# Kernel optimization log

Hardware: AMD Instinct MI355X
Metric: run time of the kernel (lower is better)

## Reference

```python
import jax, jax.numpy as jnp
import numpy as np

B, S, D_IN, D_OUT = 4, 2048, 1024, 1024

def setup_inputs() -> dict:
    key = jax.random.key(0)
    kx, kq, kk, kv = jax.random.split(key, 4)
    sc = 1.0 / np.sqrt(D_IN)
    x = jax.random.normal(kx, (B, S, D_IN), dtype=jnp.float32)
    Wq = jax.random.normal(kq, (D_IN, D_OUT), dtype=jnp.float32) * sc
    Wk = jax.random.normal(kk, (D_IN, D_OUT), dtype=jnp.float32) * sc
    Wv = jax.random.normal(kv, (D_IN, D_OUT), dtype=jnp.float32) * sc
    return {"x": x, "Wq": Wq, "Wk": Wk, "Wv": Wv}

def reference(x, Wq, Wk, Wv):
    # x: [B,S,Din]; projections to [B,S,Dout]
    q = jnp.einsum('bsd,de->bse', x, Wq)
    k = jnp.einsum('bsd,de->bse', x, Wk)
    v = jnp.einsum('bsd,de->bse', x, Wv)
    scale = 1.0 / jnp.sqrt(jnp.asarray(q.shape[-1], q.dtype))
    scores = jnp.einsum('bqe,bke->bqk', q, k) * scale  # [B,S,S]
    causal = jnp.tril(jnp.ones((scores.shape[-2], scores.shape[-1]), dtype=bool))
    scores = jnp.where(causal, scores, -jnp.inf)
    attn = jax.nn.softmax(scores, axis=-1)
    # dropout p=0.0 -> identity
    return jnp.einsum('bqk,bke->bqe', attn, v)
```

## Files before the change

kernel.cpp:

```cpp
#include <hip/hip_runtime.h>

#define SEQ 2048
#define DIM 1024

typedef __attribute__((ext_vector_type(8))) __bf16 bf16x8;
typedef __attribute__((ext_vector_type(4))) float f32x4;

typedef __attribute__((address_space(1))) unsigned char gu8_t;
typedef __attribute__((address_space(3))) unsigned char lu8_t;

__device__ __forceinline__ void async_copy16(const void* g, void* l) {
  __builtin_amdgcn_global_load_lds((gu8_t*)g, (lu8_t*)l, 16, 0, 0);
}

__device__ __forceinline__ ushort f2bf(float f) {
  union { float f; unsigned u; } v;
  v.f = f;
  unsigned r = v.u + 0x7FFFu + ((v.u >> 16) & 1u);
  return (ushort)(r >> 16);
}

__global__ void prep(const void* __restrict__ xin, const void* __restrict__ w0,
                     const void* __restrict__ w1, const void* __restrict__ w2,
                     ushort* __restrict__ xb, ushort* __restrict__ wt,
                     int* __restrict__ flag, float* __restrict__ lsum) {
  __shared__ ushort tile[64][68];
  __shared__ int redi[4];
  const int bid = blockIdx.x;
  const int t = threadIdx.x;

  const unsigned wv = ((const unsigned*)xin)[t];
  const unsigned b = (wv >> 8) & 0x7Fu;
  int hits = (b >= 0x3Bu && b <= 0x42u) ? 1 : 0;
#pragma unroll
  for (int o = 32; o > 0; o >>= 1) hits += __shfl_xor(hits, o, 64);
  if ((t & 63) == 0) redi[t >> 6] = hits;
  __syncthreads();
  const int bf = (redi[0] + redi[1] + redi[2] + redi[3] > 128) ? 1 : 0;

  if (bid >= 1280) {
    reinterpret_cast<float4*>(lsum)[(bid - 1280) * 256 + t] =
        make_float4(0.f, 0.f, 0.f, 0.f);
    if (bid == 1280 && t == 0) *flag = bf;
    return;
  }

  if (bid < 512) {
#pragma unroll
    for (int j = 0; j < 8; j++) {
      const int i = bid * 2048 + j * 256 + t;
      if (bf) {
        reinterpret_cast<uint4*>(xb)[i] =
            reinterpret_cast<const uint4*>(xin)[i];
      } else {
        const float4* f = reinterpret_cast<const float4*>(xin);
        const float4 a = f[2 * i], bb = f[2 * i + 1];
        ushort4 lo, hi;
        lo.x = f2bf(a.x); lo.y = f2bf(a.y); lo.z = f2bf(a.z); lo.w = f2bf(a.w);
        hi.x = f2bf(bb.x); hi.y = f2bf(bb.y); hi.z = f2bf(bb.z);
        hi.w = f2bf(bb.w);
        reinterpret_cast<ushort4*>(xb)[2 * i] = lo;
        reinterpret_cast<ushort4*>(xb)[2 * i + 1] = hi;
      }
    }
    return;
  }

  const int rem = bid - 512;
  const int z = rem >> 8;
  const int within = rem & 255;
  const int c0 = (within & 15) * 64, r0 = (within >> 4) * 64;
  const void* in = (z == 0) ? w0 : (z == 1) ? w1 : w2;
  ushort* op = wt + (size_t)z * 1024 * 1024;

  if (bf) {
    const ushort* ip = (const ushort*)in;
#pragma unroll
    for (int i = 0; i < 4; i++) {
      const int lin = i * 256 + t;
      const int r = lin >> 4, c4 = (lin & 15) << 2;
      const ushort4 v = *reinterpret_cast<const ushort4*>(
          ip + (size_t)(r0 + r) * 1024 + c0 + c4);
      tile[r][c4 + 0] = v.x; tile[r][c4 + 1] = v.y;
      tile[r][c4 + 2] = v.z; tile[r][c4 + 3] = v.w;
    }
  } else {
    const float* ip = (const float*)in;
#pragma unroll
    for (int i = 0; i < 4; i++) {
      const int lin = i * 256 + t;
      const int r = lin >> 4, c4 = (lin & 15) << 2;
      const float4 v = *reinterpret_cast<const float4*>(
          ip + (size_t)(r0 + r) * 1024 + c0 + c4);
      tile[r][c4 + 0] = f2bf(v.x); tile[r][c4 + 1] = f2bf(v.y);
      tile[r][c4 + 2] = f2bf(v.z); tile[r][c4 + 3] = f2bf(v.w);
    }
  }
  __syncthreads();
#pragma unroll
  for (int i = 0; i < 4; i++) {
    const int lin = i * 256 + t;
    const int c = lin >> 4, r4 = (lin & 15) << 2;
    ushort4 v;
    v.x = tile[r4 + 0][c]; v.y = tile[r4 + 1][c];
    v.z = tile[r4 + 2][c]; v.w = tile[r4 + 3][c];
    *reinterpret_cast<ushort4*>(op + (size_t)(c0 + c) * 1024 + r0 + r4) = v;
  }
}

template <int MODE>
__global__ __launch_bounds__(512, 2) void gemm8(
    const ushort* __restrict__ p0, const ushort* __restrict__ p1,
    const ushort* __restrict__ p2, void* __restrict__ c0,
    void* __restrict__ c1, float* __restrict__ lsum) {
  __shared__ ushort sA[2][2][128 * 64];
  __shared__ ushort sB[2][2][128 * 64];

  const ushort* A;
  const ushort* B;
  ushort* C;
  float* ls = nullptr;
  int m0, n0;
  long ldA, ldB, ldC;
  float scale = 1.0f;
  bool isE = false;

  const int id = blockIdx.x;
  if constexpr (MODE == 0) {
    const int z = id >> 7, r = id & 127;
    m0 = (r >> 2) << 8;
    n0 = (r & 3) << 8;
    A = p0; ldA = 1024;
    B = p1 + (size_t)z * 1024 * 1024; ldB = 1024;
    C = (ushort*)c0 + (size_t)z * 8192 * 1024; ldC = 1024;
    scale = z ? 1.0f : 0.03125f;
  } else {
    if (id < 144) {
      isE = true;
      const int z = id / 36;
      const int tri = id % 36;
      int mt = 0;
      while ((mt + 1) * (mt + 2) / 2 <= tri) mt++;
      const int nt = tri - mt * (mt + 1) / 2;
      m0 = mt << 8;
      n0 = nt << 8;
      A = p0 + (size_t)z * SEQ * DIM; ldA = 1024;
      B = p0 + (size_t)8192 * 1024 + (size_t)z * SEQ * DIM; ldB = 1024;
      C = (ushort*)c0 + (size_t)z * SEQ * SEQ; ldC = 2048;
      ls = lsum + (size_t)z * SEQ;
    } else {
      const int r = id - 144;
      m0 = (r >> 5) << 8;
      n0 = (r & 31) << 8;
      A = p1 + 2 * 1024 * 1024; ldA = 1024;
      B = p2; ldB = 1024;
      C = (ushort*)c1; ldC = 8192;
    }
  }
  constexpr int nT = 16;

  const int tid = threadIdx.x;
  const int lane = tid & 63;
  const int w = tid >> 6;
  const int quad = lane >> 4;
  const int l15 = lane & 15;
  const int ah = w >> 2;
  const int wn = (w & 3) << 6;
  const int bh = wn >> 7;
  const int bo = wn & 64;

  const ushort* aSrc[2][2];
  const ushort* bSrc[2][2];
#pragma unroll
  for (int h = 0; h < 2; h++)
#pragma unroll
    for (int i = 0; i < 2; i++) {
      const int g = i * 512 + tid;
      const int rl = g >> 3;
      const int ck = (g & 7) ^ (rl & 7);
      aSrc[h][i] = A + (size_t)(m0 + h * 128 + rl) * ldA + ck * 8;
      bSrc[h][i] = B + (size_t)(n0 + h * 128 + rl) * ldB + ck * 8;
    }

  auto stageA = [&](int t, int b) {
#pragma unroll
    for (int h = 0; h < 2; h++)
#pragma unroll
      for (int i = 0; i < 2; i++)
        async_copy16(aSrc[h][i] + t * 64, &sA[b][h][(i * 512 + tid) * 8]);
  };
  auto stageB = [&](int t, int b) {
#pragma unroll
    for (int h = 0; h < 2; h++)
#pragma unroll
      for (int i = 0; i < 2; i++)
        async_copy16(bSrc[h][i] + t * 64, &sB[b][h][(i * 512 + tid) * 8]);
  };
  auto rdA = [&](int b, int rbase, int kh) -> bf16x8 {
    const int row = rbase + l15;
    const int ck = ((kh << 2) | quad) ^ (row & 7);
    return *(const bf16x8*)&sA[b][ah][row * 64 + ck * 8];
  };
  auto rdB = [&](int b, int rbase, int kh) -> bf16x8 {
    const int row = rbase + l15;
    const int ck = ((kh << 2) | quad) ^ (row & 7);
    return *(const bf16x8*)&sB[b][bh][row * 64 + ck * 8];
  };

  f32x4 acc[8][4] = {};
  bf16x8 aF[8], bF0[4], bF1[4];

  stageA(0, 0); stageB(0, 0);
  stageA(1, 1); stageB(1, 1);
  asm volatile("s_waitcnt vmcnt(8)" ::: "memory");
  __builtin_amdgcn_s_barrier();

#pragma unroll 1
  for (int t = 0; t < nT; t++) {
    const int b = t & 1;

#pragma unroll
    for (int m = 0; m < 4; m++)
#pragma unroll
      for (int h = 0; h < 2; h++) aF[m * 2 + h] = rdA(b, m * 16, h);
#pragma unroll
    for (int n = 0; n < 2; n++)
#pragma unroll
      for (int h = 0; h < 2; h++) bF0[n * 2 + h] = rdB(b, bo + n * 16, h);
    __builtin_amdgcn_s_barrier();
    __builtin_amdgcn_s_setprio(1);
#pragma unroll
    for (int h = 0; h < 2; h++)
#pragma unroll
      for (int m = 0; m < 4; m++)
#pragma unroll
        for (int n = 0; n < 2; n++)
          acc[m][n] = __builtin_amdgcn_mfma_f32_16x16x32_bf16(
              aF[m * 2 + h], bF0[n * 2 + h], acc[m][n], 0, 0, 0);
    __builtin_amdgcn_s_setprio(0);
    __builtin_amdgcn_s_barrier();

#pragma unroll
    for (int n = 0; n < 2; n++)
#pragma unroll
      for (int h = 0; h < 2; h++)
        bF1[n * 2 + h] = rdB(b, bo + 32 + n * 16, h);
    __builtin_amdgcn_s_barrier();
    __builtin_amdgcn_s_setprio(1);
#pragma unroll
    for (int h = 0; h < 2; h++)
#pragma unroll
      for (int m = 0; m < 4; m++)
#pragma unroll
        for (int n = 0; n < 2; n++)
          acc[m][2 + n] = __builtin_amdgcn_mfma_f32_16x16x32_bf16(
              aF[m * 2 + h], bF1[n * 2 + h], acc[m][2 + n], 0, 0, 0);
    __builtin_amdgcn_s_setprio(0);
    __builtin_amdgcn_s_barrier();

#pragma unroll
    for (int m = 0; m < 4; m++)
#pragma unroll
      for (int h = 0; h < 2; h++) aF[m * 2 + h] = rdA(b, 64 + m * 16, h);
    if (t + 2 < nT) stageB(t + 2, b);
    __builtin_amdgcn_s_barrier();
    __builtin_amdgcn_s_setprio(1);
#pragma unroll
    for (int h = 0; h < 2; h++)
#pragma unroll
      for (int m = 0; m < 4; m++)
#pragma unroll
        for (int n = 0; n < 2; n++)
          acc[4 + m][n] = __builtin_amdgcn_mfma_f32_16x16x32_bf16(
              aF[m * 2 + h], bF0[n * 2 + h], acc[4 + m][n], 0, 0, 0);
    __builtin_amdgcn_s_setprio(0);
    __builtin_amdgcn_s_barrier();

    if (t + 2 < nT) stageA(t + 2, b);
    __builtin_amdgcn_s_setprio(1);
#pragma unroll
    for (int h = 0; h < 2; h++)
#pragma unroll
      for (int m = 0; m < 4; m++)
#pragma unroll
        for (int n = 0; n < 2; n++)
          acc[4 + m][2 + n] = __builtin_amdgcn_mfma_f32_16x16x32_bf16(
              aF[m * 2 + h], bF1[n * 2 + h], acc[4 + m][2 + n], 0, 0, 0);
    __builtin_amdgcn_s_setprio(0);
    if (t + 2 < nT)
      asm volatile("s_waitcnt vmcnt(8)" ::: "memory");
    else
      asm volatile("s_waitcnt vmcnt(0)" ::: "memory");
    __builtin_amdgcn_s_barrier();
  }

  if (MODE == 1 && isE) {
#pragma unroll
    for (int mi = 0; mi < 8; mi++)
#pragma unroll
      for (int r = 0; r < 4; r++) {
        const int row = m0 + ah * 128 + mi * 16 + quad * 4 + r;
        float partial = 0.0f;
#pragma unroll
        for (int ni = 0; ni < 4; ni++) {
          const int col = n0 + wn + ni * 16 + l15;
          const float ev = (col <= row) ? __expf(acc[mi][ni][r]) : 0.0f;
          C[(size_t)row * ldC + col] = f2bf(ev);
          partial += ev;
        }
#pragma unroll
        for (int o = 1; o < 16; o <<= 1) partial += __shfl_xor(partial, o, 64);
        if (l15 == 0) atomicAdd(&ls[row], partial);
      }
  } else {
#pragma unroll
    for (int mi = 0; mi < 8; mi++)
#pragma unroll
      for (int ni = 0; ni < 4; ni++)
#pragma unroll
        for (int r = 0; r < 4; r++) {
          const int row = m0 + ah * 128 + mi * 16 + quad * 4 + r;
          const int col = n0 + wn + ni * 16 + l15;
          C[(size_t)row * ldC + col] = f2bf(acc[mi][ni][r] * scale);
        }
  }
}

template <int EPI, int OUTK, int CK, int SWIZ, int M, int N, int K, long AZ,
          long BZ, long CZ, long BRS>
__global__ __launch_bounds__(256, 4) void gemm_t(
    const ushort* __restrict__ A, const ushort* __restrict__ Bt,
    void* __restrict__ Cv, const int* __restrict__ flag,
    float* __restrict__ lsum, float scale0, float scale1) {
  __shared__ ushort lA[128 * 64];
  __shared__ ushort lB[128 * 64];
  __shared__ float lsh[(EPI == 2) ? 128 : 1];

  constexpr int MT = M / 128;
  const int nT = gridDim.x;
  const int id = blockIdx.y * nT + blockIdx.x;
  const int xcd = id & 7;
  const int loc = id >> 3;
  int nt, mt;
  if constexpr (SWIZ == 1) {
    const int ng = nT >> 3;
    nt = xcd * ng + loc % ng;
    mt = loc / ng;
  } else if constexpr (SWIZ == 2) {
    if (loc <= xcd) { mt = xcd; nt = loc; }
    else { mt = MT - 1 - xcd; nt = loc - xcd - 1; }
  } else if constexpr (SWIZ == 3) {
    nt = xcd;
    mt = loc;
  } else {
    nt = loc % nT;
    mt = xcd + ((loc / nT) << 3);
  }
  const int n0 = nt * 128;
  const int m0 = mt * 128;

  const int z = blockIdx.z;
  const ushort* Ab = A + (size_t)z * AZ;
  const ushort* Bb = Bt + (size_t)z * BZ;

  const int t = threadIdx.x;
  const int lane = t & 63;
  const int w = t >> 6;
  const int wm = (w >> 1) * 64;
  const int wn = (w & 1) * 64;
  const int quad = lane >> 4;
  const int l15 = lane & 15;

  if constexpr (EPI == 2) {
    if (t < 128) lsh[t] = 1.0f / lsum[(size_t)z * M + m0 + t];
  }

  f32x4 acc[4][4] = {};

  const int kEnd = CK ? ((m0 + 128 < K) ? (m0 + 128) : K) : K;

  for (int k0 = 0; k0 < kEnd; k0 += 64) {
    __syncthreads();
#pragma unroll
    for (int g0 = 0; g0 < 1024; g0 += 256) {
      const int g = g0 + t;
      const int r = g >> 3, c = (g & 7) << 3;
      async_copy16(Ab + (size_t)(m0 + r) * K + k0 + c, lA + g * 8);
    }
#pragma unroll
    for (int g0 = 0; g0 < 1024; g0 += 256) {
      const int g = g0 + t;
      const int r = g >> 3, c = (g & 7) << 3;
      async_copy16(Bb + (size_t)(n0 + r) * BRS + k0 + c, lB + g * 8);
    }
    __syncthreads();

#pragma unroll
    for (int h = 0; h < 2; h++) {
      bf16x8 af[4], bfr[4];
#pragma unroll
      for (int mi = 0; mi < 4; mi++)
        af[mi] = *(const bf16x8*)(lA + (wm + mi * 16 + l15) * 64 + h * 32 +
                                  quad * 8);
#pragma unroll
      for (int ni = 0; ni < 4; ni++)
        bfr[ni] = *(const bf16x8*)(lB + (wn + ni * 16 + l15) * 64 + h * 32 +
                                   quad * 8);
#pragma unroll
      for (int mi = 0; mi < 4; mi++)
#pragma unroll
        for (int ni = 0; ni < 4; ni++)
          acc[mi][ni] = __builtin_amdgcn_mfma_f32_16x16x32_bf16(
              af[mi], bfr[ni], acc[mi][ni], 0, 0, 0);
    }
  }

  const size_t zc = (size_t)z * CZ;

  if constexpr (EPI == 1) {
    ushort* C = (ushort*)Cv + zc;
    float* ls = lsum + (size_t)z * M;
#pragma unroll
    for (int mi = 0; mi < 4; mi++)
#pragma unroll
      for (int r = 0; r < 4; r++) {
        const int row = m0 + wm + mi * 16 + quad * 4 + r;
        float partial = 0.0f;
#pragma unroll
        for (int ni = 0; ni < 4; ni++) {
          const int col = n0 + wn + ni * 16 + l15;
          const float ev = (col <= row) ? __expf(acc[mi][ni][r]) : 0.0f;
          C[(size_t)row * N + col] = f2bf(ev);
          partial += ev;
        }
#pragma unroll
        for (int o = 1; o < 16; o <<= 1) partial += __shfl_xor(partial, o, 64);
        if (l15 == 0) atomicAdd(&ls[row], partial);
      }
    return;
  } else {
    const float scale = (z == 0) ? scale0 : scale1;
    const bool storeBf = (OUTK == 1) || (OUTK == 2 && *flag != 0);
#pragma unroll
    for (int mi = 0; mi < 4; mi++)
#pragma unroll
      for (int ni = 0; ni < 4; ni++)
#pragma unroll
        for (int r = 0; r < 4; r++) {
          const int lrow = wm + mi * 16 + quad * 4 + r;
          const int row = m0 + lrow;
          const int col = n0 + wn + ni * 16 + l15;
          const float sc = (EPI == 2) ? lsh[lrow] : scale;
          const float vv = acc[mi][ni][r] * sc;
          if (storeBf) {
            ushort* C = (ushort*)Cv + zc;
            C[(size_t)row * N + col] = f2bf(vv);
          } else {
            float* C = (float*)Cv + zc;
            C[(size_t)row * N + col] = vv;
          }
        }
  }
}

extern "C" void kernel_launch(void* const* d_in, const int* in_sizes, int n_in,
                              void* d_out, int out_size, void* d_ws,
                              size_t ws_size, hipStream_t stream) {
  char* ws = (char*)d_ws;
  const size_t MB = 1024 * 1024;
  int* flag = (int*)ws;
  ushort* wt = (ushort*)(ws + 1 * MB);
  ushort* xb = (ushort*)(ws + 7 * MB);
  ushort* q = (ushort*)(ws + 23 * MB);
  ushort* vt = (ushort*)(ws + 55 * MB);
  ushort* sc = (ushort*)(ws + 71 * MB);
  float* lsum = (float*)(ws + 103 * MB);

  prep<<<dim3(1288), 256, 0, stream>>>(d_in[0], d_in[1], d_in[2], d_in[3], xb,
                                       wt, flag, lsum);

  gemm8<0><<<dim3(256), 512, 0, stream>>>(xb, wt, nullptr, (void*)q, nullptr,
                                          nullptr);

  gemm8<1><<<dim3(272), 512, 0, stream>>>(q, wt, xb, (void*)sc, (void*)vt,
                                          lsum);

  gemm_t<2, 2, 1, 3, 2048, 1024, 2048, (long)SEQ * SEQ, 2048L,
         (long)SEQ * DIM, 8192L>
      <<<dim3(8, 16, 4), 256, 0, stream>>>(sc, vt, d_out, flag, lsum, 1.0f,
                                           1.0f);
}
```

Before: 242.0 us.

## Fuse prep and two GEMM launches into one cooperative kernel with grid syncs

New measurement: 520.8 us. +115.2%, slower.

```diff
diff --git a/kernel.cpp b/kernel.cpp
--- a/kernel.cpp
+++ b/kernel.cpp
@@ -1,4 +1,7 @@
 #include <hip/hip_runtime.h>
+#include <hip/hip_cooperative_groups.h>
+
+namespace cg = cooperative_groups;
 
 #define SEQ 2048
 #define DIM 1024
@@ -20,143 +23,14 @@
   return (ushort)(r >> 16);
 }
 
-__global__ void prep(const void* __restrict__ xin, const void* __restrict__ w0,
-                     const void* __restrict__ w1, const void* __restrict__ w2,
-                     ushort* __restrict__ xb, ushort* __restrict__ wt,
-                     int* __restrict__ flag, float* __restrict__ lsum) {
-  __shared__ ushort tile[64][68];
-  __shared__ int redi[4];
-  const int bid = blockIdx.x;
-  const int t = threadIdx.x;
-
-  const unsigned wv = ((const unsigned*)xin)[t];
-  const unsigned b = (wv >> 8) & 0x7Fu;
-  int hits = (b >= 0x3Bu && b <= 0x42u) ? 1 : 0;
-#pragma unroll
-  for (int o = 32; o > 0; o >>= 1) hits += __shfl_xor(hits, o, 64);
-  if ((t & 63) == 0) redi[t >> 6] = hits;
-  __syncthreads();
-  const int bf = (redi[0] + redi[1] + redi[2] + redi[3] > 128) ? 1 : 0;
-
-  if (bid >= 1280) {
-    reinterpret_cast<float4*>(lsum)[(bid - 1280) * 256 + t] =
-        make_float4(0.f, 0.f, 0.f, 0.f);
-    if (bid == 1280 && t == 0) *flag = bf;
-    return;
-  }
-
-  if (bid < 512) {
-#pragma unroll
-    for (int j = 0; j < 8; j++) {
-      const int i = bid * 2048 + j * 256 + t;
-      if (bf) {
-        reinterpret_cast<uint4*>(xb)[i] =
-            reinterpret_cast<const uint4*>(xin)[i];
-      } else {
-        const float4* f = reinterpret_cast<const float4*>(xin);
-        const float4 a = f[2 * i], bb = f[2 * i + 1];
-        ushort4 lo, hi;
-        lo.x = f2bf(a.x); lo.y = f2bf(a.y); lo.z = f2bf(a.z); lo.w = f2bf(a.w);
-        hi.x = f2bf(bb.x); hi.y = f2bf(bb.y); hi.z = f2bf(bb.z);
-        hi.w = f2bf(bb.w);
-        reinterpret_cast<ushort4*>(xb)[2 * i] = lo;
-        reinterpret_cast<ushort4*>(xb)[2 * i + 1] = hi;
-      }
-    }
-    return;
-  }
-
-  const int rem = bid - 512;
-  const int z = rem >> 8;
-  const int within = rem & 255;
-  const int c0 = (within & 15) * 64, r0 = (within >> 4) * 64;
-  const void* in = (z == 0) ? w0 : (z == 1) ? w1 : w2;
-  ushort* op = wt + (size_t)z * 1024 * 1024;
-
-  if (bf) {
-    const ushort* ip = (const ushort*)in;
-#pragma unroll
-    for (int i = 0; i < 4; i++) {
-      const int lin = i * 256 + t;
-      const int r = lin >> 4, c4 = (lin & 15) << 2;
-      const ushort4 v = *reinterpret_cast<const ushort4*>(
-          ip + (size_t)(r0 + r) * 1024 + c0 + c4);
-      tile[r][c4 + 0] = v.x; tile[r][c4 + 1] = v.y;
-      tile[r][c4 + 2] = v.z; tile[r][c4 + 3] = v.w;
-    }
-  } else {
-    const float* ip = (const float*)in;
-#pragma unroll
-    for (int i = 0; i < 4; i++) {
-      const int lin = i * 256 + t;
-      const int r = lin >> 4, c4 = (lin & 15) << 2;
-      const float4 v = *reinterpret_cast<const float4*>(
-          ip + (size_t)(r0 + r) * 1024 + c0 + c4);
-      tile[r][c4 + 0] = f2bf(v.x); tile[r][c4 + 1] = f2bf(v.y);
-      tile[r][c4 + 2] = f2bf(v.z); tile[r][c4 + 3] = f2bf(v.w);
-    }
-  }
-  __syncthreads();
-#pragma unroll
-  for (int i = 0; i < 4; i++) {
-    const int lin = i * 256 + t;
-    const int c = lin >> 4, r4 = (lin & 15) << 2;
-    ushort4 v;
-    v.x = tile[r4 + 0][c]; v.y = tile[r4 + 1][c];
-    v.z = tile[r4 + 2][c]; v.w = tile[r4 + 3][c];
-    *reinterpret_cast<ushort4*>(op + (size_t)(c0 + c) * 1024 + r0 + r4) = v;
-  }
-}
-
-template <int MODE>
-__global__ __launch_bounds__(512, 2) void gemm8(
-    const ushort* __restrict__ p0, const ushort* __restrict__ p1,
-    const ushort* __restrict__ p2, void* __restrict__ c0,
-    void* __restrict__ c1, float* __restrict__ lsum) {
-  __shared__ ushort sA[2][2][128 * 64];
-  __shared__ ushort sB[2][2][128 * 64];
-
-  const ushort* A;
-  const ushort* B;
-  ushort* C;
-  float* ls = nullptr;
-  int m0, n0;
-  long ldA, ldB, ldC;
-  float scale = 1.0f;
-  bool isE = false;
-
-  const int id = blockIdx.x;
-  if constexpr (MODE == 0) {
-    const int z = id >> 7, r = id & 127;
-    m0 = (r >> 2) << 8;
-    n0 = (r & 3) << 8;
-    A = p0; ldA = 1024;
-    B = p1 + (size_t)z * 1024 * 1024; ldB = 1024;
-    C = (ushort*)c0 + (size_t)z * 8192 * 1024; ldC = 1024;
-    scale = z ? 1.0f : 0.03125f;
-  } else {
-    if (id < 144) {
-      isE = true;
-      const int z = id / 36;
-      const int tri = id % 36;
-      int mt = 0;
-      while ((mt + 1) * (mt + 2) / 2 <= tri) mt++;
-      const int nt = tri - mt * (mt + 1) / 2;
-      m0 = mt << 8;
-      n0 = nt << 8;
-      A = p0 + (size_t)z * SEQ * DIM; ldA = 1024;
-      B = p0 + (size_t)8192 * 1024 + (size_t)z * SEQ * DIM; ldB = 1024;
-      C = (ushort*)c0 + (size_t)z * SEQ * SEQ; ldC = 2048;
-      ls = lsum + (size_t)z * SEQ;
-    } else {
-      const int r = id - 144;
-      m0 = (r >> 5) << 8;
-      n0 = (r & 31) << 8;
-      A = p1 + 2 * 1024 * 1024; ldA = 1024;
-      B = p2; ldB = 1024;
-      C = (ushort*)c1; ldC = 8192;
-    }
-  }
+__device__ __forceinline__ void gemm_core(
+    const ushort* __restrict__ A, const ushort* __restrict__ B,
+    ushort* __restrict__ C, float* __restrict__ ls, const bool isE,
+    const int m0, const int n0, const long ldA, const long ldB,
+    const long ldC, const float scale) {
+  __shared__ ushort sA[2][2][8192];
+  __shared__ ushort sB[2][2][8192];
+
   constexpr int nT = 16;
 
   const int tid = threadIdx.x;
@@ -294,7 +168,7 @@
     __builtin_amdgcn_s_barrier();
   }
 
-  if (MODE == 1 && isE) {
+  if (isE) {
 #pragma unroll
     for (int mi = 0; mi < 8; mi++)
 #pragma unroll
@@ -323,6 +197,138 @@
           const int col = n0 + wn + ni * 16 + l15;
           C[(size_t)row * ldC + col] = f2bf(acc[mi][ni][r] * scale);
         }
+  }
+}
+
+__global__ __launch_bounds__(512, 2) void fused(
+    const void* __restrict__ xin, const void* __restrict__ w0,
+    const void* __restrict__ w1, const void* __restrict__ w2,
+    ushort* __restrict__ xb, ushort* __restrict__ wt, int* __restrict__ flag,
+    float* __restrict__ lsum, ushort* __restrict__ q, ushort* __restrict__ sc,
+    ushort* __restrict__ vt) {
+  __shared__ ushort tile[64][68];
+  __shared__ int redi[8];
+  const int bid = blockIdx.x;
+  const int tid = threadIdx.x;
+  cg::grid_group grid = cg::this_grid();
+
+  {
+    const unsigned wv = ((const unsigned*)xin)[tid];
+    const unsigned b1 = (wv >> 8) & 0x7Fu;
+    int hits = (b1 >= 0x3Bu && b1 <= 0x42u) ? 1 : 0;
+#pragma unroll
+    for (int o = 32; o > 0; o >>= 1) hits += __shfl_xor(hits, o, 64);
+    if ((tid & 63) == 0) redi[tid >> 6] = hits;
+  }
+  __syncthreads();
+  int hsum = 0;
+#pragma unroll
+  for (int i = 0; i < 8; i++) hsum += redi[i];
+  const int bf = (hsum > 256) ? 1 : 0;
+
+  if (bid == 0 && tid == 0) *flag = bf;
+  if (bid < 4)
+    reinterpret_cast<float4*>(lsum)[bid * 512 + tid] =
+        make_float4(0.f, 0.f, 0.f, 0.f);
+
+  if (bf) {
+#pragma unroll
+    for (int j = 0; j < 8; j++) {
+      const int i = bid * 4096 + j * 512 + tid;
+      reinterpret_cast<uint4*>(xb)[i] = reinterpret_cast<const uint4*>(xin)[i];
+    }
+  } else {
+#pragma unroll
+    for (int j = 0; j < 8; j++) {
+      const int i = bid * 4096 + j * 512 + tid;
+      const float4* f = reinterpret_cast<const float4*>(xin);
+      const float4 a = f[2 * i], bb = f[2 * i + 1];
+      ushort4 lo, hi;
+      lo.x = f2bf(a.x); lo.y = f2bf(a.y); lo.z = f2bf(a.z); lo.w = f2bf(a.w);
+      hi.x = f2bf(bb.x); hi.y = f2bf(bb.y); hi.z = f2bf(bb.z);
+      hi.w = f2bf(bb.w);
+      reinterpret_cast<ushort4*>(xb)[2 * i] = lo;
+      reinterpret_cast<ushort4*>(xb)[2 * i + 1] = hi;
+    }
+  }
+
+#pragma unroll 1
+  for (int tt = 0; tt < 3; tt++) {
+    const int rem = bid * 3 + tt;
+    const int z = rem >> 8;
+    const int within = rem & 255;
+    const int c0 = (within & 15) * 64, r0 = (within >> 4) * 64;
+    const void* in = (z == 0) ? w0 : (z == 1) ? w1 : w2;
+    ushort* op = wt + (size_t)z * 1048576;
+
+    __syncthreads();
+    if (bf) {
+      const ushort* ip = (const ushort*)in;
+#pragma unroll
+      for (int i = 0; i < 2; i++) {
+        const int lin = i * 512 + tid;
+        const int r = lin >> 4, c4 = (lin & 15) << 2;
+        const ushort4 v = *reinterpret_cast<const ushort4*>(
+            ip + (size_t)(r0 + r) * 1024 + c0 + c4);
+        tile[r][c4 + 0] = v.x; tile[r][c4 + 1] = v.y;
+        tile[r][c4 + 2] = v.z; tile[r][c4 + 3] = v.w;
+      }
+    } else {
+      const float* ip = (const float*)in;
+#pragma unroll
+      for (int i = 0; i < 2; i++) {
+        const int lin = i * 512 + tid;
+        const int r = lin >> 4, c4 = (lin & 15) << 2;
+        const float4 v = *reinterpret_cast<const float4*>(
+            ip + (size_t)(r0 + r) * 1024 + c0 + c4);
+        tile[r][c4 + 0] = f2bf(v.x); tile[r][c4 + 1] = f2bf(v.y);
+        tile[r][c4 + 2] = f2bf(v.z); tile[r][c4 + 3] = f2bf(v.w);
+      }
+    }
+    __syncthreads();
+#pragma unroll
+    for (int i = 0; i < 2; i++) {
+      const int lin = i * 512 + tid;
+      const int c = lin >> 4, r4 = (lin & 15) << 2;
+      ushort4 v;
+      v.x = tile[r4 + 0][c]; v.y = tile[r4 + 1][c];
+      v.z = tile[r4 + 2][c]; v.w = tile[r4 + 3][c];
+      *reinterpret_cast<ushort4*>(op + (size_t)(c0 + c) * 1024 + r0 + r4) = v;
+    }
+  }
+
+  __threadfence();
+  grid.sync();
+  __threadfence();
+
+  {
+    const int z = bid >> 7, r = bid & 127;
+    gemm_core(xb, wt + (size_t)z * 1048576, q + (size_t)z * 8388608, nullptr,
+              false, (r >> 2) << 8, (r & 3) << 8, 1024, 1024, 1024,
+              z ? 1.0f : 0.03125f);
+  }
+
+  __threadfence();
+  grid.sync();
+  __threadfence();
+
+#pragma unroll 1
+  for (int u = bid; u < 272; u += 256) {
+    if (u < 144) {
+      const int z = u / 36;
+      const int tri = u % 36;
+      int mt = 0;
+      while ((mt + 1) * (mt + 2) / 2 <= tri) mt++;
+      const int nt = tri - mt * (mt + 1) / 2;
+      gemm_core(q + (size_t)z * SEQ * DIM,
+                q + 8388608 + (size_t)z * SEQ * DIM,
+                sc + (size_t)z * SEQ * SEQ, lsum + (size_t)z * SEQ, true,
+                mt << 8, nt << 8, 1024, 1024, 2048, 1.0f);
+    } else {
+      const int r = u - 144;
+      gemm_core(wt + 2097152, xb, vt, nullptr, false, (r >> 5) << 8,
+                (r & 31) << 8, 1024, 1024, 8192, 1.0f);
+    }
   }
 }
 
@@ -476,14 +482,15 @@
   ushort* sc = (ushort*)(ws + 71 * MB);
   float* lsum = (float*)(ws + 103 * MB);
 
-  prep<<<dim3(1288), 256, 0, stream>>>(d_in[0], d_in[1], d_in[2], d_in[3], xb,
-                                       wt, flag, lsum);
-
-  gemm8<0><<<dim3(256), 512, 0, stream>>>(xb, wt, nullptr, (void*)q, nullptr,
-                                          nullptr);
-
-  gemm8<1><<<dim3(272), 512, 0, stream>>>(q, wt, xb, (void*)sc, (void*)vt,
-                                          lsum);
+  const void* x0 = d_in[0];
+  const void* w0p = d_in[1];
+  const void* w1p = d_in[2];
+  const void* w2p = d_in[3];
+  void* args[] = {(void*)&x0,  (void*)&w0p, (void*)&w1p, (void*)&w2p,
+                  (void*)&xb,  (void*)&wt,  (void*)&flag, (void*)&lsum,
+                  (void*)&q,   (void*)&sc,  (void*)&vt};
+  hipLaunchCooperativeKernel(reinterpret_cast<void*>(fused), dim3(256),
+                             dim3(512), args, 0, stream);
 
   gemm_t<2, 2, 1, 3, 2048, 1024, 2048, (long)SEQ * SEQ, 2048L,
          (long)SEQ * DIM, 8192L>
```
